# Optimization experiments

Measured on AMD Instinct MI355X. Metric: run time of the kernel, lower is better.

The kernel has to match this reference:

```python
import jax, jax.numpy as jnp
import numpy as np

T, B, DI, DL, V = 1024, 128, 256, 512, 10000


def setup_inputs() -> dict:
    key = jax.random.key(0)
    ks = jax.random.split(key, 6)
    return {
        "X": jax.random.randint(ks[0], (T, B), 0, V, dtype=jnp.int64),
        "h0": jnp.zeros((B, DL), dtype=jnp.float32),
        "emb": jax.random.normal(ks[1], (V, DI), dtype=jnp.float32),
        "Wi": jax.random.normal(ks[2], (DI, DL), dtype=jnp.float32) * (1.0 / np.sqrt(DI)),
        "bi": jax.random.normal(ks[3], (DL,), dtype=jnp.float32) * 0.02,
        "Wh": jax.random.normal(ks[4], (DL, DL), dtype=jnp.float32) * (1.0 / np.sqrt(DL)),
        "bh": jax.random.normal(ks[5], (DL,), dtype=jnp.float32) * 0.02,
    }


def reference(X, h0, emb, Wi, bi, Wh, bh):
    # Elman RNN: h_t = tanh(W_i emb(x_t) + b_i + W_h h_{t-1} + b_h)
    Xe = emb[X]                              # [T, B, DI] embedding lookup
    pre = jnp.einsum("tbd,dl->tbl", Xe, Wi) + bi  # input projections, batched over time

    def step(h, p):
        h_new = jnp.tanh(p + h @ Wh + bh)
        return h_new, h_new

    _, H = jax.lax.scan(step, h0, pre)       # H: [T, B, DL]
    return H
```

## Files before the change

kernel.cpp:

```cpp
#include <hip/hip_runtime.h>
#include <math.h>

typedef _Float16 f16;
typedef _Float16 f16x8 __attribute__((ext_vector_type(8)));
typedef float f32x4 __attribute__((ext_vector_type(4)));

#define T_ 1024
#define B_ 128
#define DI_ 256
#define DL_ 512
#define V_ 10000

#define OFF_EMBH   0u
#define OFF_WIT    5120000u
#define OFF_WHT    5382144u
#define OFF_BSUM   5906432u
#define OFF_FLAGS  5908480u

__global__ void prep_emb_k(const float* __restrict__ emb, f16* __restrict__ embH, int n) {
  for (int i = blockIdx.x * blockDim.x + threadIdx.x; i < n; i += gridDim.x * blockDim.x)
    embH[i] = (f16)emb[i];
}

__global__ void prep_w_k(const float* __restrict__ Wi, const float* __restrict__ Wh,
                         const float* __restrict__ bi, const float* __restrict__ bh,
                         f16* __restrict__ WiT, f16* __restrict__ WhT,
                         float* __restrict__ bsum) {
  int i = blockIdx.x * blockDim.x + threadIdx.x;
  if (i < 131072) {
    int n = i & 511, k = i >> 9;
    WiT[n * 256 + k] = (f16)Wi[k * 512 + n];
  } else if (i < 131072 + 262144) {
    int s = i - 131072;
    int n = s & 511, k = s >> 9;
    WhT[n * 512 + k] = (f16)Wh[k * 512 + n];
  } else if (i < 131072 + 262144 + 512) {
    int s = i - 131072 - 262144;
    bsum[s] = bi[s] + bh[s];
  }
}

__global__ __launch_bounds__(256) void gemmA_k(
    const int* __restrict__ X, const f16* __restrict__ embH,
    const f16* __restrict__ WiT, const float* __restrict__ bsum,
    float* __restrict__ out) {
  __shared__ f16 Ah[128][40];
  __shared__ f16 Bh[128][40];
  __shared__ int idxL[128];

  int tid = threadIdx.x;
  int lane = tid & 63, w = tid >> 6;
  int wr = w >> 1, wc = w & 1;
  int m0 = blockIdx.y * 128, n0 = blockIdx.x * 128;

  if (tid < 128) {
    int v = X[m0 + tid];
    idxL[tid] = (v < 0) ? 0 : ((v >= V_) ? (V_ - 1) : v);
  }
  __syncthreads();

  f32x4 acc[4][4];
#pragma unroll
  for (int i = 0; i < 4; i++)
#pragma unroll
    for (int jj = 0; jj < 4; jj++) acc[i][jj] = (f32x4){0.f, 0.f, 0.f, 0.f};

  int ar = lane & 15, koff = (lane >> 4) * 8;

  for (int kk = 0; kk < 8; kk++) {
    int k0 = kk * 32;
#pragma unroll
    for (int q = 0; q < 2; q++) {
      int s = tid + 256 * q;
      int row = s >> 2, part = s & 3;
      *(uint4*)&Ah[row][part * 8] = *(const uint4*)&embH[idxL[row] * 256 + k0 + part * 8];
      *(uint4*)&Bh[row][part * 8] = *(const uint4*)&WiT[(n0 + row) * 256 + k0 + part * 8];
    }
    __syncthreads();
    f16x8 a[4], b[4];
#pragma unroll
    for (int i = 0; i < 4; i++) a[i] = *(const f16x8*)&Ah[wr * 64 + i * 16 + ar][koff];
#pragma unroll
    for (int jj = 0; jj < 4; jj++) b[jj] = *(const f16x8*)&Bh[wc * 64 + jj * 16 + ar][koff];
#pragma unroll
    for (int i = 0; i < 4; i++)
#pragma unroll
      for (int jj = 0; jj < 4; jj++)
        acc[i][jj] = __builtin_amdgcn_mfma_f32_16x16x32_f16(a[i], b[jj], acc[i][jj], 0, 0, 0);
    __syncthreads();
  }

  int r0 = (lane >> 4) * 4;
#pragma unroll
  for (int i = 0; i < 4; i++) {
#pragma unroll
    for (int jj = 0; jj < 4; jj++) {
      int gm = m0 + wr * 64 + i * 16 + r0;
      int gn = n0 + wc * 64 + jj * 16 + ar;
      float bs = bsum[gn];
#pragma unroll
      for (int r = 0; r < 4; r++)
        out[(size_t)(gm + r) * 512 + gn] = acc[i][jj][r] + bs;
    }
  }
}

__global__ __launch_bounds__(256, 1) void rnnB_k(
    const float* __restrict__ h0, const f16* __restrict__ WhT,
    float* __restrict__ H, int* flags) {
  __shared__ f16 WhL[128][520];
  __shared__ f16 hL[16][520];

  int tid = threadIdx.x, lane = tid & 63, w = tid >> 6;
  int bid = blockIdx.x;
  int c = bid & 7;
  int j = bid >> 3;
  int b0 = c * 16, n0 = j * 128;

  for (int s = tid; s < 128 * 64; s += 256) {
    int r = s >> 6, part = s & 63;
    *(uint4*)&WhL[r][part * 8] = *(const uint4*)&WhT[(size_t)(n0 + r) * 512 + part * 8];
  }

  int ar = lane & 15, koff = (lane >> 4) * 8;
  int r0 = (lane >> 4) * 4;

  for (int t = 0; t < 1024; t++) {
    float* Ht = H + (size_t)t * (B_ * DL_);

    int gcol0 = n0 + w * 32 + ar;
    float pre[2][4];
#pragma unroll
    for (int jj = 0; jj < 2; jj++)
#pragma unroll
      for (int r = 0; r < 4; r++)
        pre[jj][r] = Ht[(size_t)(b0 + r0 + r) * 512 + gcol0 + jj * 16];

    if (t > 0 && tid < 4 && tid != j) {
      while (__hip_atomic_load(&flags[c * 4 + tid], __ATOMIC_ACQUIRE,
                               __HIP_MEMORY_SCOPE_AGENT) < t) {
      }
    }
    __syncthreads();

    const float4* hs = (const float4*)((t == 0) ? (h0 + b0 * 512)
                                                : (H + (size_t)(t - 1) * (B_ * DL_) + b0 * 512));
#pragma unroll
    for (int q = 0; q < 8; q++) {
      int s = tid + 256 * q;
      float4 v = hs[s];
      int row = s >> 7, k4 = (s & 127) * 4;
      hL[row][k4 + 0] = (f16)v.x;
      hL[row][k4 + 1] = (f16)v.y;
      hL[row][k4 + 2] = (f16)v.z;
      hL[row][k4 + 3] = (f16)v.w;
    }
    __syncthreads();

    f32x4 acc0 = {0.f, 0.f, 0.f, 0.f}, acc1 = {0.f, 0.f, 0.f, 0.f};
#pragma unroll
    for (int kk = 0; kk < 16; kk++) {
      f16x8 a = *(const f16x8*)&hL[ar][kk * 32 + koff];
      f16x8 bv0 = *(const f16x8*)&WhL[w * 32 + ar][kk * 32 + koff];
      f16x8 bv1 = *(const f16x8*)&WhL[w * 32 + 16 + ar][kk * 32 + koff];
      acc0 = __builtin_amdgcn_mfma_f32_16x16x32_f16(a, bv0, acc0, 0, 0, 0);
      acc1 = __builtin_amdgcn_mfma_f32_16x16x32_f16(a, bv1, acc1, 0, 0, 0);
    }

#pragma unroll
    for (int jj = 0; jj < 2; jj++) {
      f32x4 acc = jj ? acc1 : acc0;
#pragma unroll
      for (int r = 0; r < 4; r++) {
        size_t o = (size_t)(b0 + r0 + r) * 512 + gcol0 + jj * 16;
        Ht[o] = tanhf(acc[r] + pre[jj][r]);
      }
    }

    __syncthreads();
    if (tid == 0)
      __hip_atomic_store(&flags[c * 4 + j], t + 1, __ATOMIC_RELEASE,
                         __HIP_MEMORY_SCOPE_AGENT);
  }
}

extern "C" void kernel_launch(void* const* d_in, const int* in_sizes, int n_in,
                              void* d_out, int out_size, void* d_ws, size_t ws_size,
                              hipStream_t stream) {
  const int* X     = (const int*)d_in[0];
  const float* h0  = (const float*)d_in[1];
  const float* emb = (const float*)d_in[2];
  const float* Wi  = (const float*)d_in[3];
  const float* bi  = (const float*)d_in[4];
  const float* Wh  = (const float*)d_in[5];
  const float* bh  = (const float*)d_in[6];
  float* H = (float*)d_out;

  char* ws = (char*)d_ws;
  f16* embH   = (f16*)(ws + OFF_EMBH);
  f16* WiT    = (f16*)(ws + OFF_WIT);
  f16* WhT    = (f16*)(ws + OFF_WHT);
  float* bsum = (float*)(ws + OFF_BSUM);
  int* flags  = (int*)(ws + OFF_FLAGS);

  hipMemsetAsync(flags, 0, 32 * sizeof(int), stream);
  prep_emb_k<<<2560, 256, 0, stream>>>(emb, embH, V_ * DI_);
  prep_w_k<<<1538, 256, 0, stream>>>(Wi, Wh, bi, bh, WiT, WhT, bsum);
  gemmA_k<<<dim3(4, 1024), 256, 0, stream>>>(X, embH, WiT, bsum, H);
  rnnB_k<<<32, 256, 0, stream>>>(h0, WhT, H, flags);
}
```

Before: 3.610 ms.

## Exchange recurrent state via fp16 double buffer with relaxed cache-bypass sync

Each step's new hidden slice is written in fp16 to a double-buffered exchange area using cache-bypassing stores. Peers then read only the three remote 128-column slices, while the block's own slice is written straight into shared memory. Flag synchronisation becomes relaxed system-scope atomics with a bounded spin, and tanhf is replaced by an exp2/rcp approximation. The aim is to cut per-step latency on the serial recurrence chain (fp32 reload, conversion, acquire/release fences). The risks are weaker memory-ordering guarantees, a spin timeout that could silently read stale data, and slightly lower tanh accuracy.

```diff
diff --git a/kernel.cpp b/kernel.cpp
--- a/kernel.cpp
+++ b/kernel.cpp
@@ -16,6 +16,13 @@
 #define OFF_WHT    5382144u
 #define OFF_BSUM   5906432u
 #define OFF_FLAGS  5908480u
+#define OFF_XBUF   5908608u
+
+__device__ __forceinline__ float fast_tanh(float x) {
+  float xx = fminf(fmaxf(x, -10.f), 10.f);
+  float e = __builtin_amdgcn_exp2f(xx * 2.88539008177793f);
+  return 1.f - 2.f * __builtin_amdgcn_rcpf(e + 1.f);
+}
 
 __global__ void prep_emb_k(const float* __restrict__ emb, f16* __restrict__ embH, int n) {
   for (int i = blockIdx.x * blockDim.x + threadIdx.x; i < n; i += gridDim.x * blockDim.x)
@@ -107,7 +114,7 @@
 
 __global__ __launch_bounds__(256, 1) void rnnB_k(
     const float* __restrict__ h0, const f16* __restrict__ WhT,
-    float* __restrict__ H, int* flags) {
+    float* __restrict__ H, int* flags, f16* xbuf) {
   __shared__ f16 WhL[128][520];
   __shared__ f16 hL[16][520];
 
@@ -124,11 +131,15 @@
 
   int ar = lane & 15, koff = (lane >> 4) * 8;
   int r0 = (lane >> 4) * 4;
+  int gcol0 = n0 + w * 32 + ar;
+
+  int srow = tid >> 4, spart = tid & 15;
+  int sb[3];
+  { int q = 0; for (int bb = 0; bb < 4; bb++) if (bb != j) sb[q++] = bb; }
 
   for (int t = 0; t < 1024; t++) {
     float* Ht = H + (size_t)t * (B_ * DL_);
 
-    int gcol0 = n0 + w * 32 + ar;
     float pre[2][4];
 #pragma unroll
     for (int jj = 0; jj < 2; jj++)
@@ -136,24 +147,42 @@
       for (int r = 0; r < 4; r++)
         pre[jj][r] = Ht[(size_t)(b0 + r0 + r) * 512 + gcol0 + jj * 16];
 
-    if (t > 0 && tid < 4 && tid != j) {
-      while (__hip_atomic_load(&flags[c * 4 + tid], __ATOMIC_ACQUIRE,
-                               __HIP_MEMORY_SCOPE_AGENT) < t) {
-      }
-    }
-    __syncthreads();
-
-    const float4* hs = (const float4*)((t == 0) ? (h0 + b0 * 512)
-                                                : (H + (size_t)(t - 1) * (B_ * DL_) + b0 * 512));
-#pragma unroll
-    for (int q = 0; q < 8; q++) {
-      int s = tid + 256 * q;
-      float4 v = hs[s];
-      int row = s >> 7, k4 = (s & 127) * 4;
-      hL[row][k4 + 0] = (f16)v.x;
-      hL[row][k4 + 1] = (f16)v.y;
-      hL[row][k4 + 2] = (f16)v.z;
-      hL[row][k4 + 3] = (f16)v.w;
+    if (t > 0) {
+#pragma unroll
+      for (int s = 0; s < 3; s++) {
+        const int* fp = &flags[c * 4 + sb[s]];
+        int spin = 0;
+        while (__hip_atomic_load(fp, __ATOMIC_RELAXED, __HIP_MEMORY_SCOPE_SYSTEM) < t) {
+          if (++spin > (1 << 26)) break;
+        }
+      }
+      asm volatile("" ::: "memory");
+
+      const f16* xb = xbuf + ((size_t)((t - 1) & 1) * 8 + c) * (16 * 512);
+      const f16* base = xb + srow * 512;
+      const f16* p0 = base + sb[0] * 128 + spart * 8;
+      const f16* p1 = base + sb[1] * 128 + spart * 8;
+      const f16* p2 = base + sb[2] * 128 + spart * 8;
+      uint4 v0, v1, v2;
+      asm volatile("global_load_dwordx4 %0, %1, off sc0 sc1" : "=v"(v0) : "v"(p0) : "memory");
+      asm volatile("global_load_dwordx4 %0, %1, off sc0 sc1" : "=v"(v1) : "v"(p1) : "memory");
+      asm volatile("global_load_dwordx4 %0, %1, off sc0 sc1" : "=v"(v2) : "v"(p2) : "memory");
+      asm volatile("s_waitcnt vmcnt(0)" ::: "memory");
+      __builtin_amdgcn_sched_barrier(0);
+      *(uint4*)&hL[srow][sb[0] * 128 + spart * 8] = v0;
+      *(uint4*)&hL[srow][sb[1] * 128 + spart * 8] = v1;
+      *(uint4*)&hL[srow][sb[2] * 128 + spart * 8] = v2;
+    } else {
+#pragma unroll
+      for (int q = 0; q < 8; q++) {
+        int s = tid + 256 * q;
+        float4 v = ((const float4*)(h0 + b0 * 512))[s];
+        int row = s >> 7, k4 = (s & 127) * 4;
+        hL[row][k4 + 0] = (f16)v.x;
+        hL[row][k4 + 1] = (f16)v.y;
+        hL[row][k4 + 2] = (f16)v.z;
+        hL[row][k4 + 3] = (f16)v.w;
+      }
     }
     __syncthreads();
 
@@ -167,20 +196,46 @@
       acc1 = __builtin_amdgcn_mfma_f32_16x16x32_f16(a, bv1, acc1, 0, 0, 0);
     }
 
+    float hf[2][4];
+    f16 hv[2][4];
 #pragma unroll
     for (int jj = 0; jj < 2; jj++) {
       f32x4 acc = jj ? acc1 : acc0;
 #pragma unroll
       for (int r = 0; r < 4; r++) {
-        size_t o = (size_t)(b0 + r0 + r) * 512 + gcol0 + jj * 16;
-        Ht[o] = tanhf(acc[r] + pre[jj][r]);
-      }
-    }
-
-    __syncthreads();
+        hf[jj][r] = fast_tanh(acc[r] + pre[jj][r]);
+        hv[jj][r] = (f16)hf[jj][r];
+      }
+    }
+
+    f16* xw = xbuf + ((size_t)(t & 1) * 8 + c) * (16 * 512);
+#pragma unroll
+    for (int jj = 0; jj < 2; jj++)
+#pragma unroll
+      for (int r = 0; r < 4; r++) {
+        const f16* dst = xw + (r0 + r) * 512 + gcol0 + jj * 16;
+        int ui = (int)__builtin_bit_cast(unsigned short, hv[jj][r]);
+        asm volatile("global_store_short %0, %1, off sc0 sc1" :: "v"(dst), "v"(ui) : "memory");
+      }
+
+#pragma unroll
+    for (int jj = 0; jj < 2; jj++)
+#pragma unroll
+      for (int r = 0; r < 4; r++)
+        Ht[(size_t)(b0 + r0 + r) * 512 + gcol0 + jj * 16] = hf[jj][r];
+
+    asm volatile("s_waitcnt vmcnt(0)" ::: "memory");
+    __syncthreads();
+
+#pragma unroll
+    for (int jj = 0; jj < 2; jj++)
+#pragma unroll
+      for (int r = 0; r < 4; r++)
+        hL[r0 + r][gcol0 + jj * 16] = hv[jj][r];
+
     if (tid == 0)
-      __hip_atomic_store(&flags[c * 4 + j], t + 1, __ATOMIC_RELEASE,
-                         __HIP_MEMORY_SCOPE_AGENT);
+      __hip_atomic_store(&flags[c * 4 + j], t + 1, __ATOMIC_RELAXED,
+                         __HIP_MEMORY_SCOPE_SYSTEM);
   }
 }
 
@@ -202,10 +257,11 @@
   f16* WhT    = (f16*)(ws + OFF_WHT);
   float* bsum = (float*)(ws + OFF_BSUM);
   int* flags  = (int*)(ws + OFF_FLAGS);
+  f16* xbuf   = (f16*)(ws + OFF_XBUF);
 
   hipMemsetAsync(flags, 0, 32 * sizeof(int), stream);
   prep_emb_k<<<2560, 256, 0, stream>>>(emb, embH, V_ * DI_);
   prep_w_k<<<1538, 256, 0, stream>>>(Wi, Wh, bi, bh, WiT, WhT, bsum);
   gemmA_k<<<dim3(4, 1024), 256, 0, stream>>>(X, embH, WiT, bsum, H);
-  rnnB_k<<<32, 256, 0, stream>>>(h0, WhT, H, flags);
-}
+  rnnB_k<<<32, 256, 0, stream>>>(h0, WhT, H, flags, xbuf);
+}
```

Measured after the change: 3.352 ms. 1.08x faster.

## Make each RNN block own a batch slice to remove inter-block flag sync

Applied to the files above, without the earlier changes.

The recurrent kernel now runs 8 blocks, each owning 16 batch rows across all 512 hidden columns. This removes the per-timestep cross-block atomic flag polling and the global round-trip for h, since the new h is written straight back into LDS in MFMA fragment order. Wh is pre-packed into fragment layout and split across registers, LDS and streamed global loads. The input projection is written in fragment order so the next step's pre-activations can be prefetched with vector loads, and tanh is replaced with an exp2/rcp approximation. The trade-off is that only 8 CUs are used and register pressure is high.

```diff
diff --git a/kernel.cpp b/kernel.cpp
--- a/kernel.cpp
+++ b/kernel.cpp
@@ -13,9 +13,14 @@
 
 #define OFF_EMBH   0u
 #define OFF_WIT    5120000u
-#define OFF_WHT    5382144u
+#define OFF_WFRAG  5382144u
 #define OFF_BSUM   5906432u
-#define OFF_FLAGS  5908480u
+
+__device__ __forceinline__ float fast_tanh(float x) {
+  float xx = fminf(fmaxf(x, -10.f), 10.f);
+  float e = __builtin_amdgcn_exp2f(xx * 2.88539008177793f);
+  return 1.f - 2.f * __builtin_amdgcn_rcpf(e + 1.f);
+}
 
 __global__ void prep_emb_k(const float* __restrict__ emb, f16* __restrict__ embH, int n) {
   for (int i = blockIdx.x * blockDim.x + threadIdx.x; i < n; i += gridDim.x * blockDim.x)
@@ -24,18 +29,23 @@
 
 __global__ void prep_w_k(const float* __restrict__ Wi, const float* __restrict__ Wh,
                          const float* __restrict__ bi, const float* __restrict__ bh,
-                         f16* __restrict__ WiT, f16* __restrict__ WhT,
+                         f16* __restrict__ WiT, f16* __restrict__ Wfrag,
                          float* __restrict__ bsum) {
   int i = blockIdx.x * blockDim.x + threadIdx.x;
   if (i < 131072) {
     int n = i & 511, k = i >> 9;
     WiT[n * 256 + k] = (f16)Wi[k * 512 + n];
-  } else if (i < 131072 + 262144) {
+  } else if (i < 131072 + 32768) {
     int s = i - 131072;
-    int n = s & 511, k = s >> 9;
-    WhT[n * 512 + k] = (f16)Wh[k * 512 + n];
-  } else if (i < 131072 + 262144 + 512) {
-    int s = i - 131072 - 262144;
+    int l = s & 63, kk = (s >> 6) & 15, ct = s >> 10;
+    int n = ct * 16 + (l & 15);
+    int kbase = kk * 32 + (l >> 4) * 8;
+    f16 tmp[8];
+#pragma unroll
+    for (int e = 0; e < 8; e++) tmp[e] = (f16)Wh[(size_t)(kbase + e) * 512 + n];
+    *(f16x8*)&Wfrag[(size_t)s * 8] = *(f16x8*)tmp;
+  } else if (i < 131072 + 32768 + 512) {
+    int s = i - 131072 - 32768;
     bsum[s] = bi[s] + bh[s];
   }
 }
@@ -51,7 +61,8 @@
   int tid = threadIdx.x;
   int lane = tid & 63, w = tid >> 6;
   int wr = w >> 1, wc = w & 1;
-  int m0 = blockIdx.y * 128, n0 = blockIdx.x * 128;
+  int by = blockIdx.y, bx = blockIdx.x;
+  int m0 = by * 128, n0 = bx * 128;
 
   if (tid < 128) {
     int v = X[m0 + tid];
@@ -90,97 +101,113 @@
     __syncthreads();
   }
 
-  int r0 = (lane >> 4) * 4;
 #pragma unroll
   for (int i = 0; i < 4; i++) {
 #pragma unroll
     for (int jj = 0; jj < 4; jj++) {
-      int gm = m0 + wr * 64 + i * 16 + r0;
-      int gn = n0 + wc * 64 + jj * 16 + ar;
-      float bs = bsum[gn];
-#pragma unroll
-      for (int r = 0; r < 4; r++)
-        out[(size_t)(gm + r) * 512 + gn] = acc[i][jj][r] + bs;
+      int c = wr * 4 + i;
+      int ct = bx * 8 + wc * 4 + jj;
+      float bs = bsum[ct * 16 + ar];
+      f32x4 v = acc[i][jj];
+      v[0] += bs; v[1] += bs; v[2] += bs; v[3] += bs;
+      *(f32x4*)&out[(size_t)by * 65536 + (size_t)c * 8192 + ct * 256 + lane * 4] = v;
     }
   }
 }
 
 __global__ __launch_bounds__(256, 1) void rnnB_k(
-    const float* __restrict__ h0, const f16* __restrict__ WhT,
-    float* __restrict__ H, int* flags) {
-  __shared__ f16 WhL[128][520];
-  __shared__ f16 hL[16][520];
+    const float* __restrict__ h0, const f16* __restrict__ Wfrag,
+    float* __restrict__ H) {
+  __shared__ f16 Wlds[8 * 16 * 64 * 8];
+  __shared__ f16 hA[16 * 64 * 8];
 
   int tid = threadIdx.x, lane = tid & 63, w = tid >> 6;
-  int bid = blockIdx.x;
-  int c = bid & 7;
-  int j = bid >> 3;
-  int b0 = c * 16, n0 = j * 128;
-
-  for (int s = tid; s < 128 * 64; s += 256) {
-    int r = s >> 6, part = s & 63;
-    *(uint4*)&WhL[r][part * 8] = *(const uint4*)&WhT[(size_t)(n0 + r) * 512 + part * 8];
-  }
-
-  int ar = lane & 15, koff = (lane >> 4) * 8;
-  int r0 = (lane >> 4) * 4;
+  int c = blockIdx.x;
+  int w8 = w * 8;
+  int ar = lane & 15, r0 = (lane >> 4) * 4;
+
+  const f16x8* Wfr = (const f16x8*)Wfrag;
+
+  for (int idx = tid; idx < 8192; idx += 256) {
+    int l = idx & 63, kk = (idx >> 6) & 15, s = idx >> 10;
+    int ts = (s >> 1) * 8 + 4 + (s & 1);
+    *(f16x8*)&Wlds[(size_t)idx * 8] = Wfr[(ts * 16 + kk) * 64 + l];
+  }
+  for (int idx = tid; idx < 8192; idx += 256) {
+    int kk = idx >> 9, l = (idx >> 3) & 63, e = idx & 7;
+    int row = l & 15, k = kk * 32 + (l >> 4) * 8 + e;
+    hA[idx] = (f16)h0[(size_t)(c * 16 + row) * 512 + k];
+  }
+
+  f16x8 Wreg[64];
+#pragma unroll
+  for (int ti = 0; ti < 4; ti++)
+#pragma unroll
+    for (int kk = 0; kk < 16; kk++)
+      Wreg[ti * 16 + kk] = Wfr[((w8 + ti) * 16 + kk) * 64 + lane];
+
+  int s6base = (w8 + 6) * 16 * 64 + lane;
+  int s7base = (w8 + 7) * 16 * 64 + lane;
+  int sl0 = w * 2, sl1 = w * 2 + 1;
+
+  f16x8 ws6[2], ws7[2];
+  ws6[0] = Wfr[s6base];
+  ws7[0] = Wfr[s7base];
+  f32x4 pre[8];
+  {
+    const f32x4* preb = (const f32x4*)(H + (size_t)c * 8192);
+#pragma unroll
+    for (int ti = 0; ti < 8; ti++) pre[ti] = preb[(w8 + ti) * 64 + lane];
+  }
 
   for (int t = 0; t < 1024; t++) {
-    float* Ht = H + (size_t)t * (B_ * DL_);
-
-    int gcol0 = n0 + w * 32 + ar;
-    float pre[2][4];
-#pragma unroll
-    for (int jj = 0; jj < 2; jj++)
-#pragma unroll
-      for (int r = 0; r < 4; r++)
-        pre[jj][r] = Ht[(size_t)(b0 + r0 + r) * 512 + gcol0 + jj * 16];
-
-    if (t > 0 && tid < 4 && tid != j) {
-      while (__hip_atomic_load(&flags[c * 4 + tid], __ATOMIC_ACQUIRE,
-                               __HIP_MEMORY_SCOPE_AGENT) < t) {
+    __syncthreads();
+
+    f32x4 acc[8];
+#pragma unroll
+    for (int ti = 0; ti < 8; ti++) acc[ti] = (f32x4){0.f, 0.f, 0.f, 0.f};
+
+#pragma unroll
+    for (int kk = 0; kk < 16; kk++) {
+      f16x8 a = *(const f16x8*)&hA[(size_t)(kk * 64 + lane) * 8];
+      if (kk < 15) {
+        ws6[(kk + 1) & 1] = Wfr[s6base + (kk + 1) * 64];
+        ws7[(kk + 1) & 1] = Wfr[s7base + (kk + 1) * 64];
       }
-    }
-    __syncthreads();
-
-    const float4* hs = (const float4*)((t == 0) ? (h0 + b0 * 512)
-                                                : (H + (size_t)(t - 1) * (B_ * DL_) + b0 * 512));
-#pragma unroll
-    for (int q = 0; q < 8; q++) {
-      int s = tid + 256 * q;
-      float4 v = hs[s];
-      int row = s >> 7, k4 = (s & 127) * 4;
-      hL[row][k4 + 0] = (f16)v.x;
-      hL[row][k4 + 1] = (f16)v.y;
-      hL[row][k4 + 2] = (f16)v.z;
-      hL[row][k4 + 3] = (f16)v.w;
-    }
-    __syncthreads();
-
-    f32x4 acc0 = {0.f, 0.f, 0.f, 0.f}, acc1 = {0.f, 0.f, 0.f, 0.f};
-#pragma unroll
-    for (int kk = 0; kk < 16; kk++) {
-      f16x8 a = *(const f16x8*)&hL[ar][kk * 32 + koff];
-      f16x8 bv0 = *(const f16x8*)&WhL[w * 32 + ar][kk * 32 + koff];
-      f16x8 bv1 = *(const f16x8*)&WhL[w * 32 + 16 + ar][kk * 32 + koff];
-      acc0 = __builtin_amdgcn_mfma_f32_16x16x32_f16(a, bv0, acc0, 0, 0, 0);
-      acc1 = __builtin_amdgcn_mfma_f32_16x16x32_f16(a, bv1, acc1, 0, 0, 0);
-    }
-
-#pragma unroll
-    for (int jj = 0; jj < 2; jj++) {
-      f32x4 acc = jj ? acc1 : acc0;
+      acc[0] = __builtin_amdgcn_mfma_f32_16x16x32_f16(a, Wreg[0 * 16 + kk], acc[0], 0, 0, 0);
+      acc[1] = __builtin_amdgcn_mfma_f32_16x16x32_f16(a, Wreg[1 * 16 + kk], acc[1], 0, 0, 0);
+      acc[2] = __builtin_amdgcn_mfma_f32_16x16x32_f16(a, Wreg[2 * 16 + kk], acc[2], 0, 0, 0);
+      acc[3] = __builtin_amdgcn_mfma_f32_16x16x32_f16(a, Wreg[3 * 16 + kk], acc[3], 0, 0, 0);
+      f16x8 w4 = *(const f16x8*)&Wlds[(size_t)((sl0 * 16 + kk) * 64 + lane) * 8];
+      f16x8 w5 = *(const f16x8*)&Wlds[(size_t)((sl1 * 16 + kk) * 64 + lane) * 8];
+      acc[4] = __builtin_amdgcn_mfma_f32_16x16x32_f16(a, w4, acc[4], 0, 0, 0);
+      acc[5] = __builtin_amdgcn_mfma_f32_16x16x32_f16(a, w5, acc[5], 0, 0, 0);
+      acc[6] = __builtin_amdgcn_mfma_f32_16x16x32_f16(a, ws6[kk & 1], acc[6], 0, 0, 0);
+      acc[7] = __builtin_amdgcn_mfma_f32_16x16x32_f16(a, ws7[kk & 1], acc[7], 0, 0, 0);
+    }
+
+    __syncthreads();
+
+    float* Hblk = H + (size_t)t * 65536 + (size_t)c * 8192;
+#pragma unroll
+    for (int ti = 0; ti < 8; ti++) {
+      int ct = w8 + ti;
+      int kkA = ct >> 1;
 #pragma unroll
       for (int r = 0; r < 4; r++) {
-        size_t o = (size_t)(b0 + r0 + r) * 512 + gcol0 + jj * 16;
-        Ht[o] = tanhf(acc[r] + pre[jj][r]);
+        float v = fast_tanh(acc[ti][r] + pre[ti][r]);
+        Hblk[(size_t)(r0 + r) * 512 + ct * 16 + ar] = v;
+        int lA = (r0 + r) | ((((ct & 1) << 1) | (ar >> 3)) << 4);
+        hA[((kkA * 64 + lA) << 3) + (ar & 7)] = (f16)v;
       }
     }
 
-    __syncthreads();
-    if (tid == 0)
-      __hip_atomic_store(&flags[c * 4 + j], t + 1, __ATOMIC_RELEASE,
-                         __HIP_MEMORY_SCOPE_AGENT);
+    int tn = (t < 1023) ? t + 1 : 0;
+    const f32x4* preb = (const f32x4*)(H + (size_t)tn * 65536 + (size_t)c * 8192);
+#pragma unroll
+    for (int ti = 0; ti < 8; ti++) pre[ti] = preb[(w8 + ti) * 64 + lane];
+    ws6[0] = Wfr[s6base];
+    ws7[0] = Wfr[s7base];
   }
 }
 
@@ -199,13 +226,11 @@
   char* ws = (char*)d_ws;
   f16* embH   = (f16*)(ws + OFF_EMBH);
   f16* WiT    = (f16*)(ws + OFF_WIT);
-  f16* WhT    = (f16*)(ws + OFF_WHT);
+  f16* Wfrag  = (f16*)(ws + OFF_WFRAG);
   float* bsum = (float*)(ws + OFF_BSUM);
-  int* flags  = (int*)(ws + OFF_FLAGS);
-
-  hipMemsetAsync(flags, 0, 32 * sizeof(int), stream);
+
   prep_emb_k<<<2560, 256, 0, stream>>>(emb, embH, V_ * DI_);
-  prep_w_k<<<1538, 256, 0, stream>>>(Wi, Wh, bi, bh, WiT, WhT, bsum);
+  prep_w_k<<<642, 256, 0, stream>>>(Wi, Wh, bi, bh, WiT, Wfrag, bsum);
   gemmA_k<<<dim3(4, 1024), 256, 0, stream>>>(X, embH, WiT, bsum, H);
-  rnnB_k<<<32, 256, 0, stream>>>(h0, WhT, H, flags);
-}
+  rnnB_k<<<8, 256, 0, stream>>>(h0, Wfrag, H);
+}
```

Measured after the change: 5.570 ms. 54.3% more time.
